# Optimization experiments

Measured on AMD Instinct MI355X. Metric: run time of the kernel, lower is better.

Reference implementation:

```python
import jax, jax.numpy as jnp
import numpy as np

N_NODES = 100000
N_EDGES = 1600000
IN_FEATS = 64
N_CLASSES = 64


def setup_inputs() -> dict:
    key = jax.random.key(0)
    k1, k2, k3, k4, k5 = jax.random.split(key, 5)
    feat = jax.random.normal(k1, (N_NODES, IN_FEATS), dtype=jnp.float32)
    edge_row = jnp.sort(jax.random.randint(k2, (N_EDGES,), 0, N_NODES))
    edge_col = jax.random.randint(k3, (N_EDGES,), 0, N_NODES)
    # values of the cached normalized adjacency power (all positive, ~1/deg scale)
    edge_val = jax.random.uniform(k4, (N_EDGES,), dtype=jnp.float32) / 16.0
    # nn.Linear(in_feats, n_classes): weight [C, F] (xavier), bias zeros
    limit = float(np.sqrt(6.0 / (IN_FEATS + N_CLASSES)))
    W = jax.random.uniform(k5, (N_CLASSES, IN_FEATS), dtype=jnp.float32,
                           minval=-limit, maxval=limit)
    b = jnp.zeros((N_CLASSES,), dtype=jnp.float32)
    return {"feat": feat, "edge_row": edge_row, "edge_col": edge_col,
            "edge_val": edge_val, "W": W, "b": b}


def reference(feat, edge_row, edge_col, edge_val, W, b):
    # SpMM: h = A_pre @ feat, A_pre given as COO (edge_row, edge_col, edge_val)
    msg = edge_val[:, None] * feat[edge_col]          # [E, F] gather + scale
    h = jax.ops.segment_sum(msg, edge_row, num_segments=N_NODES)  # [N, F]
    # fc: Linear(in_feats -> n_classes), norm=None so no normalization
    return h @ W.T + b                                 # [N, C]
```

## Files before the change

kernel.cpp:

```cpp
#include <hip/hip_runtime.h>
#include <hip/hip_bf16.h>

typedef __attribute__((ext_vector_type(8))) short short8;
typedef __attribute__((ext_vector_type(4))) float f32x4;

__device__ __forceinline__ unsigned short f2bf(float x) {
    unsigned int u = __float_as_uint(x);
    unsigned int lsb = (u >> 16) & 1u;
    u += 0x7fffu + lsb;
    return (unsigned short)(u >> 16);
}

__device__ __forceinline__ float bf2f(unsigned int b16) {
    return __uint_as_float(b16 << 16);
}

__device__ __forceinline__ short8 pack8(f32x4 a, f32x4 b) {
    short8 r;
    r[0] = (short)f2bf(a.x); r[1] = (short)f2bf(a.y);
    r[2] = (short)f2bf(a.z); r[3] = (short)f2bf(a.w);
    r[4] = (short)f2bf(b.x); r[5] = (short)f2bf(b.y);
    r[6] = (short)f2bf(b.z); r[7] = (short)f2bf(b.w);
    return r;
}

__global__ __launch_bounds__(256) void k_init(const float* __restrict__ bias,
                                              float* __restrict__ out, long total4) {
    long i4 = (long)blockIdx.x * 256 + threadIdx.x;
    if (i4 < total4) {
        const f32x4* b4 = (const f32x4*)bias;
        ((f32x4*)out)[i4] = b4[i4 & 15];
    }
}

__global__ __launch_bounds__(256) void k_setup(const float* __restrict__ feat,
                                               const float* __restrict__ W,
                                               const float* __restrict__ bias,
                                               unsigned short* __restrict__ G,
                                               float* __restrict__ out,
                                               int N, int gblocks) {
    if ((int)blockIdx.x >= gblocks) {
        long i4 = (long)(blockIdx.x - gblocks) * 256 + threadIdx.x;
        long total4 = (long)N * 16;
        if (i4 < total4) {
            const f32x4* b4 = (const f32x4*)bias;
            ((f32x4*)out)[i4] = b4[i4 & 15];
        }
        return;
    }

    int wave = blockIdx.x * 4 + (threadIdx.x >> 6);
    int lane = threadIdx.x & 63;
    int m0 = wave * 16;
    if (m0 >= N) return;
    int n = lane & 15;
    int quad = lane >> 4;

    short8 bf[4][2];
#pragma unroll
    for (int ct = 0; ct < 4; ++ct)
#pragma unroll
        for (int ks = 0; ks < 2; ++ks) {
            const f32x4* wp = (const f32x4*)(W + (size_t)(ct * 16 + n) * 64 + ks * 32 + quad * 8);
            f32x4 w0 = wp[0];
            f32x4 w1 = wp[1];
            bf[ct][ks] = pack8(w0, w1);
        }

    int mrow = m0 + n; if (mrow >= N) mrow = N - 1;
    short8 af[2];
#pragma unroll
    for (int ks = 0; ks < 2; ++ks) {
        const f32x4* ap = (const f32x4*)(feat + (size_t)mrow * 64 + ks * 32 + quad * 8);
        f32x4 a0 = __builtin_nontemporal_load(ap);
        f32x4 a1 = __builtin_nontemporal_load(ap + 1);
        af[ks] = pack8(a0, a1);
    }

    f32x4 acc[4];
#pragma unroll
    for (int ct = 0; ct < 4; ++ct) {
        acc[ct] = (f32x4){0.f, 0.f, 0.f, 0.f};
#pragma unroll
        for (int ks = 0; ks < 2; ++ks)
            acc[ct] = __builtin_amdgcn_mfma_f32_16x16x32_bf16(af[ks], bf[ct][ks], acc[ct], 0, 0, 0);
    }

#pragma unroll
    for (int ct = 0; ct < 4; ++ct)
#pragma unroll
        for (int r = 0; r < 4; ++r) {
            int rowm = m0 + quad * 4 + r;
            if (rowm < N)
                G[(size_t)rowm * 64 + ct * 16 + n] = f2bf(acc[ct][r]);
        }
}

__global__ __launch_bounds__(256) void k_spmm(const unsigned short* __restrict__ G,
                                              const int* __restrict__ erow,
                                              const int* __restrict__ ecol,
                                              const float* __restrict__ evalv,
                                              float* __restrict__ out,
                                              int E, int cpw) {
    int wave = blockIdx.x * 4 + (threadIdx.x >> 6);
    int lane = threadIdx.x & 63;
    long base0 = (long)wave * cpw * 64;
    if (base0 >= E) return;

    int cur = __builtin_amdgcn_readfirstlane(erow[base0]);
    float acc = 0.f;

    for (int ch = 0; ch < cpw; ++ch) {
        long base = base0 + (long)ch * 64;
        if (base >= E) break;
        long idx = base + lane;
        long cidx = idx < E ? idx : (long)(E - 1);
        int rv = __builtin_nontemporal_load(erow + cidx);
        int cv = __builtin_nontemporal_load(ecol + cidx);
        float vf = (idx < E) ? __builtin_nontemporal_load(evalv + cidx) : 0.f;
        int vv = __float_as_int(vf);

#pragma unroll
        for (int j0 = 0; j0 < 64; j0 += 16) {
            float g[16];
#pragma unroll
            for (int u = 0; u < 16; ++u) {
                int c = __builtin_amdgcn_readlane(cv, j0 + u);
                g[u] = bf2f(G[((size_t)(unsigned)c << 6) | (unsigned)lane]);
            }
#pragma unroll
            for (int u = 0; u < 16; ++u) {
                int r = __builtin_amdgcn_readlane(rv, j0 + u);
                float v = __int_as_float(__builtin_amdgcn_readlane(vv, j0 + u));
                if (r != cur) {
                    atomicAdd(out + ((size_t)(unsigned)cur << 6) + lane, acc);
                    acc = 0.f;
                    cur = r;
                }
                acc = fmaf(v, g[u], acc);
            }
        }
    }
    atomicAdd(out + ((size_t)(unsigned)cur << 6) + lane, acc);
}

__global__ __launch_bounds__(256) void k_fused(const float* __restrict__ feat,
                                               const int* __restrict__ erow,
                                               const int* __restrict__ ecol,
                                               const float* __restrict__ evalv,
                                               const float* __restrict__ W,
                                               float* __restrict__ out,
                                               int E, int epw) {
    __shared__ float Wt[64 * 64];
    for (int i = threadIdx.x; i < 4096; i += 256) {
        int c = i >> 6, f = i & 63;
        Wt[f * 64 + c] = W[i];
    }
    __syncthreads();

    int wave = blockIdx.x * 4 + (threadIdx.x >> 6);
    int lane = threadIdx.x & 63;
    long e0 = (long)wave * epw;
    if (e0 >= E) return;
    long e1 = e0 + epw; if (e1 > E) e1 = E;

    int cur = erow[e0];
    float acc = 0.f;
    for (long e = e0; e < e1; ++e) {
        int r = erow[e];
        int c = ecol[e];
        float v = evalv[e];
        float g = feat[((size_t)c << 6) | lane];
        if (r != cur) {
            float res = 0.f;
#pragma unroll
            for (int f = 0; f < 64; ++f)
                res += __shfl(acc, f, 64) * Wt[f * 64 + lane];
            atomicAdd(out + ((size_t)cur << 6) + lane, res);
            acc = 0.f;
            cur = r;
        }
        acc += v * g;
    }
    {
        float res = 0.f;
#pragma unroll
        for (int f = 0; f < 64; ++f)
            res += __shfl(acc, f, 64) * Wt[f * 64 + lane];
        atomicAdd(out + ((size_t)cur << 6) + lane, res);
    }
}

extern "C" void kernel_launch(void* const* d_in, const int* in_sizes, int n_in,
                              void* d_out, int out_size, void* d_ws, size_t ws_size,
                              hipStream_t stream) {
    const float* feat  = (const float*)d_in[0];
    const int*   erow  = (const int*)d_in[1];
    const int*   ecol  = (const int*)d_in[2];
    const float* evalv = (const float*)d_in[3];
    const float* W     = (const float*)d_in[4];
    const float* bias  = (const float*)d_in[5];
    float* out = (float*)d_out;

    int N = in_sizes[0] / 64;
    int E = in_sizes[1];

    size_t need = (size_t)N * 64 * sizeof(unsigned short);
    if (ws_size >= need) {
        unsigned short* G = (unsigned short*)d_ws;
        int tiles = (N + 15) / 16;
        int gblocks = (tiles + 3) / 4;
        long total4 = (long)N * 16;
        int iblocks = (int)((total4 + 255) / 256);
        k_setup<<<gblocks + iblocks, 256, 0, stream>>>(feat, W, bias, G, out, N, gblocks);

        const int cpw = 2;
        int nchunks = (E + 63) / 64;
        int nwaves = (nchunks + cpw - 1) / cpw;
        int nblocks = (nwaves + 3) / 4;
        k_spmm<<<nblocks, 256, 0, stream>>>(G, erow, ecol, evalv, out, E, cpw);
    } else {
        long total4 = (long)N * 16;
        k_init<<<(int)((total4 + 255) / 256), 256, 0, stream>>>(bias, out, total4);
        int epw = (E + 8191) / 8192;
        if (epw < 32) epw = 32;
        int nwaves = (E + epw - 1) / epw;
        int nblocks = (nwaves + 3) / 4;
        k_fused<<<nblocks, 256, 0, stream>>>(feat, erow, ecol, evalv, W, out, E, epw);
    }
}
```

Before: 142.5 us.

## Replace interior-row atomics with plain stores and load edge indices as scalars

Each wave now covers a fixed 128 edges and reads row, column and value directly with wave-uniform addresses, so they can become scalar loads instead of per-lane loads broadcast with readlane. Rows that lie wholly inside one wave's edge range are written with a plain store of bias plus the accumulated sum, replacing an atomic add. Only the first and last row segments of each wave still use atomics. The setup kernel still initialises the whole output with bias, so that work remains even though interior rows are now overwritten.

After: 247.5 us. +73.7%, slower.

```diff
diff --git a/kernel.cpp b/kernel.cpp
--- a/kernel.cpp
+++ b/kernel.cpp
@@ -3,6 +3,8 @@
 
 typedef __attribute__((ext_vector_type(8))) short short8;
 typedef __attribute__((ext_vector_type(4))) float f32x4;
+
+#define EPW 128
 
 __device__ __forceinline__ unsigned short f2bf(float x) {
     unsigned int u = __float_as_uint(x);
@@ -100,47 +102,73 @@
                                               const int* __restrict__ erow,
                                               const int* __restrict__ ecol,
                                               const float* __restrict__ evalv,
-                                              float* __restrict__ out,
-                                              int E, int cpw) {
-    int wave = blockIdx.x * 4 + (threadIdx.x >> 6);
+                                              const float* __restrict__ bias,
+                                              float* __restrict__ out, int E) {
+    int wid = __builtin_amdgcn_readfirstlane(blockIdx.x * 4 + (threadIdx.x >> 6));
     int lane = threadIdx.x & 63;
-    long base0 = (long)wave * cpw * 64;
-    if (base0 >= E) return;
-
-    int cur = __builtin_amdgcn_readfirstlane(erow[base0]);
+    long e0 = (long)wid * EPW;
+    if (e0 >= E) return;
+    long rem = E - e0;
+    int nav = rem < EPW ? (int)rem : EPW;
+
+    float blane = bias[lane];
+    int cur = erow[e0];
     float acc = 0.f;
-
-    for (int ch = 0; ch < cpw; ++ch) {
-        long base = base0 + (long)ch * 64;
-        if (base >= E) break;
-        long idx = base + lane;
-        long cidx = idx < E ? idx : (long)(E - 1);
-        int rv = __builtin_nontemporal_load(erow + cidx);
-        int cv = __builtin_nontemporal_load(ecol + cidx);
-        float vf = (idx < E) ? __builtin_nontemporal_load(evalv + cidx) : 0.f;
-        int vv = __float_as_int(vf);
-
-#pragma unroll
-        for (int j0 = 0; j0 < 64; j0 += 16) {
-            float g[16];
-#pragma unroll
-            for (int u = 0; u < 16; ++u) {
-                int c = __builtin_amdgcn_readlane(cv, j0 + u);
-                g[u] = bf2f(G[((size_t)(unsigned)c << 6) | (unsigned)lane]);
+    bool first = true;
+
+#define CHUNK16(JB)                                                            \
+    {                                                                          \
+        int cc[16];                                                            \
+        _Pragma("unroll")                                                      \
+        for (int u = 0; u < 16; ++u) cc[u] = ecol[e0 + (JB) + u];              \
+        unsigned short gv[16];                                                 \
+        _Pragma("unroll")                                                      \
+        for (int u = 0; u < 16; ++u)                                           \
+            gv[u] = G[((size_t)(unsigned)cc[u] << 6) | (unsigned)lane];        \
+        _Pragma("unroll")                                                      \
+        for (int u = 0; u < 16; ++u) {                                         \
+            int r = erow[e0 + (JB) + u];                                       \
+            float v = evalv[e0 + (JB) + u];                                    \
+            if (r != cur) {                                                    \
+                if (first) {                                                   \
+                    atomicAdd(out + ((size_t)(unsigned)cur << 6) + lane, acc); \
+                    first = false;                                             \
+                } else {                                                       \
+                    out[((size_t)(unsigned)cur << 6) + lane] = blane + acc;    \
+                }                                                              \
+                acc = 0.f;                                                     \
+                cur = r;                                                       \
+            }                                                                  \
+            acc = fmaf(v, bf2f(gv[u]), acc);                                   \
+        }                                                                      \
+    }
+
+    if (nav == EPW) {
+#pragma unroll
+        for (int jb = 0; jb < EPW; jb += 16) CHUNK16(jb)
+    } else {
+        int j = 0;
+        for (; j + 16 <= nav; j += 16) CHUNK16(j)
+        for (; j < nav; ++j) {
+            int r = erow[e0 + j];
+            int c = ecol[e0 + j];
+            float v = evalv[e0 + j];
+            float g = bf2f(G[((size_t)(unsigned)c << 6) | (unsigned)lane]);
+            if (r != cur) {
+                if (first) {
+                    atomicAdd(out + ((size_t)(unsigned)cur << 6) + lane, acc);
+                    first = false;
+                } else {
+                    out[((size_t)(unsigned)cur << 6) + lane] = blane + acc;
+                }
+                acc = 0.f;
+                cur = r;
             }
-#pragma unroll
-            for (int u = 0; u < 16; ++u) {
-                int r = __builtin_amdgcn_readlane(rv, j0 + u);
-                float v = __int_as_float(__builtin_amdgcn_readlane(vv, j0 + u));
-                if (r != cur) {
-                    atomicAdd(out + ((size_t)(unsigned)cur << 6) + lane, acc);
-                    acc = 0.f;
-                    cur = r;
-                }
-                acc = fmaf(v, g[u], acc);
-            }
-        }
-    }
+            acc = fmaf(v, g, acc);
+        }
+    }
+#undef CHUNK16
+
     atomicAdd(out + ((size_t)(unsigned)cur << 6) + lane, acc);
 }
 
@@ -214,11 +242,9 @@
         int iblocks = (int)((total4 + 255) / 256);
         k_setup<<<gblocks + iblocks, 256, 0, stream>>>(feat, W, bias, G, out, N, gblocks);
 
-        const int cpw = 2;
-        int nchunks = (E + 63) / 64;
-        int nwaves = (nchunks + cpw - 1) / cpw;
+        int nwaves = (E + EPW - 1) / EPW;
         int nblocks = (nwaves + 3) / 4;
-        k_spmm<<<nblocks, 256, 0, stream>>>(G, erow, ecol, evalv, out, E, cpw);
+        k_spmm<<<nblocks, 256, 0, stream>>>(G, erow, ecol, evalv, bias, out, E);
     } else {
         long total4 = (long)N * 16;
         k_init<<<(int)((total4 + 255) / 256), 256, 0, stream>>>(bias, out, total4);
```
